# Kernel tuning notes

Hardware: AMD Instinct MI355X
Metric: run time of the kernel (lower is better)

Reference implementation:

```python
import jax, jax.numpy as jnp
import numpy as np

S, B, I, H = 96, 32, 64, 256


def setup_inputs() -> dict:
    key = jax.random.key(0)
    ks = jax.random.split(key, 10)
    wscale = 1.0 / np.sqrt(H)
    xscale = 1.0 / np.sqrt(I)
    return {
        "x": jax.random.normal(ks[0], (S, B, I), dtype=jnp.float32),
        # nn.Linear convention: y = x @ W.T + b, W has shape (out, in)
        "W_fx": jax.random.normal(ks[1], (H, I), dtype=jnp.float32) * xscale,
        "b_fx": jax.random.normal(ks[2], (H,), dtype=jnp.float32) * xscale,
        "W_fh": jax.random.normal(ks[3], (H, H), dtype=jnp.float32) * wscale,
        "b_fh": jax.random.normal(ks[4], (H,), dtype=jnp.float32) * wscale,
        "W_cx": jax.random.normal(ks[5], (H, I), dtype=jnp.float32) * xscale,
        "b_cx": jax.random.normal(ks[6], (H,), dtype=jnp.float32) * xscale,
        "W_ch": jax.random.normal(ks[7], (H, H), dtype=jnp.float32) * wscale,
        "b_ch": jax.random.normal(ks[8], (H,), dtype=jnp.float32) * wscale,
    }


def reference(x, W_fx, b_fx, W_fh, b_fh, W_cx, b_cx, W_ch, b_ch):
    """Faithful translation of the (buggy) torch forward.

    All three gates are the same sigmoid(f_x(x[t]) + f_h(h)) -- original reuses
    f_x/f_h for input/output gates. The candidate uses c_x(x) on the FULL
    sequence (not x[t]), so state broadcasts to (S, B, H) and h_seq is
    (S, S, B, H). Initial zero h/c are pre-broadcast to (S, B, H); since they
    are zeros this yields identical values to torch's scalar-shape init.
    """
    s, b, _ = x.shape
    h = W_fh.shape[0]
    # precompute the input projections once (same math, loop-invariant)
    fx = jnp.einsum('sbi,hi->sbh', x, W_fx) + b_fx   # (S,B,H), per-step slice
    cx = jnp.einsum('sbi,hi->sbh', x, W_cx) + b_cx   # (S,B,H), used whole every step (bug)

    def step(carry, fx_t):
        hh, cc = carry                                # each (S,B,H)
        g = jax.nn.sigmoid(fx_t + jnp.einsum('sbh,kh->sbk', hh, W_fh) + b_fh)
        cand = jnp.tanh(cx + jnp.einsum('sbh,kh->sbk', hh, W_ch) + b_ch)
        cc = g * cc + g * cand                        # forget==input gate
        hh = g * jnp.tanh(cc)                         # output gate == g
        return (hh, cc), hh

    h0 = jnp.zeros((s, b, h), dtype=x.dtype)
    (h_fin, c_fin), h_seq = jax.lax.scan(step, (h0, h0), fx)
    return h_seq, h_fin, c_fin
```

## Files before the change

kernel.cpp:

```cpp
#include <hip/hip_runtime.h>
#include <cmath>

#define S 96
#define BB 32
#define II 64
#define H 256
#define ROWS (S*BB)
#define R 16
#define NB (ROWS/R)
#define NT 512
#define PADK 272

#define FX_OFF 0
#define CX_OFF (ROWS*H)
#define WREP_OFF (2*ROWS*H)

typedef __attribute__((ext_vector_type(8))) _Float16 f16x8;
typedef __attribute__((ext_vector_type(4))) _Float16 f16x4;
typedef __attribute__((ext_vector_type(4))) float f32x4;
typedef unsigned short ushort_t;

__device__ inline ushort_t h2u(_Float16 h){ return __builtin_bit_cast(ushort_t, h); }

__device__ inline float sigm_fast(float x){
    return __builtin_amdgcn_rcpf(1.f + __expf(-x));
}
__device__ inline float tanh_fast(float x){
    return 1.f - 2.f*__builtin_amdgcn_rcpf(1.f + __expf(2.f*x));
}

__global__ void proj_kernel(const float* __restrict__ x,
                            const float* __restrict__ W_fx, const float* __restrict__ b_fx,
                            const float* __restrict__ W_cx, const float* __restrict__ b_cx,
                            const float* __restrict__ b_fh, const float* __restrict__ b_ch,
                            float* __restrict__ fx, float* __restrict__ cx)
{
    const int row = blockIdx.x;
    const int k = threadIdx.x;
    __shared__ float xs[II];
    if (k < II) xs[k] = x[row*II + k];
    __syncthreads();
    const float4* wf = reinterpret_cast<const float4*>(W_fx + k*II);
    const float4* wc = reinterpret_cast<const float4*>(W_cx + k*II);
    float af = 0.f, ac = 0.f;
#pragma unroll
    for (int i = 0; i < II/4; ++i) {
        float4 a = wf[i];
        float4 b = wc[i];
        const float* xp = &xs[i*4];
        af = fmaf(a.x, xp[0], fmaf(a.y, xp[1], fmaf(a.z, xp[2], fmaf(a.w, xp[3], af))));
        ac = fmaf(b.x, xp[0], fmaf(b.y, xp[1], fmaf(b.z, xp[2], fmaf(b.w, xp[3], ac))));
    }
    fx[row*H + k] = af + b_fx[k] + b_fh[k];
    cx[row*H + k] = ac + b_cx[k] + b_ch[k];
}

__global__ void repack_kernel(const float* __restrict__ Wf, const float* __restrict__ Wc,
                              ushort_t* __restrict__ wr)
{
    const int idx = blockIdx.x*256 + threadIdx.x;
    const int n = idx >> 8, k = idx & 255;
    const int lane = (((k >> 3) & 3) << 4) | (n & 15);
    const int dst = ((((n >> 4)*8 + (k >> 5))*64) + lane)*8 + (k & 7);
    wr[dst]         = h2u((_Float16)Wf[n*H + k]);
    wr[65536 + dst] = h2u((_Float16)Wc[n*H + k]);
}

__global__ __launch_bounds__(NT, 2) void lstm_mfma_kernel(
    const float* __restrict__ fx, const float* __restrict__ cx,
    const ushort_t* __restrict__ wr,
    float* __restrict__ out)
{
    const int tid = threadIdx.x;
    const int w = tid >> 6, lane = tid & 63;
    const int m = lane & 15, q = lane >> 4;
    const int b = blockIdx.x & 31;
    const int s0 = (blockIdx.x >> 5) * R;

    __shared__ ushort_t hh[2][2][R][PADK];

    for (int i = tid; i < 2*2*R*PADK; i += NT) (&hh[0][0][0][0])[i] = 0;

    f16x8 wF[2][8], wC[2][8];
#pragma unroll
    for (int ti = 0; ti < 2; ++ti)
#pragma unroll
        for (int kt = 0; kt < 8; ++kt) {
            const int fo = (((w*2 + ti)*8 + kt)*64 + lane)*8;
            wF[ti][kt] = *(const f16x8*)&wr[fo];
            wC[ti][kt] = *(const f16x8*)&wr[65536 + fo];
        }

    int col0[2];
    col0[0] = (w*2)*16 + q*4;
    col0[1] = (w*2 + 1)*16 + q*4;

    const int row = s0 + m;
    f32x4 cxr[2], cst[2];
#pragma unroll
    for (int ti = 0; ti < 2; ++ti) {
        cxr[ti] = *(const f32x4*)&cx[(row*BB + b)*H + col0[ti]];
        cst[ti] = (f32x4){0.f, 0.f, 0.f, 0.f};
    }

    float* hseq = out;
    float* hfin = out + (size_t)S*ROWS*H;
    float* cfin = hfin + (size_t)ROWS*H;

    const float* fxp = fx + b*H;
    float* op[2];
#pragma unroll
    for (int ti = 0; ti < 2; ++ti)
        op[ti] = hseq + ((size_t)row*BB + b)*H + col0[ti];

    __syncthreads();

    f32x4 fxv[2] = { *(const f32x4*)&fxp[col0[0]], *(const f32x4*)&fxp[col0[1]] };

#define LSTM_MFMA_TI(P, ti, accFti, accCti) do { \
    _Pragma("unroll") \
    for (int kt = 0; kt < 8; ++kt) { \
        f16x8 aH = *(const f16x8*)&hh[P][0][m][kt*32 + q*8]; \
        f16x8 aL = *(const f16x8*)&hh[P][1][m][kt*32 + q*8]; \
        accFti = __builtin_amdgcn_mfma_f32_16x16x32_f16(wF[ti][kt], aH, accFti, 0, 0, 0); \
        accFti = __builtin_amdgcn_mfma_f32_16x16x32_f16(wF[ti][kt], aL, accFti, 0, 0, 0); \
        accCti = __builtin_amdgcn_mfma_f32_16x16x32_f16(wC[ti][kt], aH, accCti, 0, 0, 0); \
        accCti = __builtin_amdgcn_mfma_f32_16x16x32_f16(wC[ti][kt], aL, accCti, 0, 0, 0); \
    } \
} while (0)

#define LSTM_EW_TI(P, ti, accFti, accCti, IS_LAST) do { \
    f32x4 hnv, cnv; \
    _Pragma("unroll") \
    for (int j = 0; j < 4; ++j) { \
        const float g    = sigm_fast(accFti[j] + fxv[ti][j]); \
        const float cand = tanh_fast(accCti[j] + cxr[ti][j]); \
        const float cn = g*(cst[ti][j] + cand); \
        cnv[j] = cn; \
        hnv[j] = g*tanh_fast(cn); \
    } \
    cst[ti] = cnv; \
    *(f32x4*)op[ti] = hnv; op[ti] += (size_t)S*BB*H; \
    f16x4 hi4, lo4; \
    _Pragma("unroll") \
    for (int j = 0; j < 4; ++j) { \
        hi4[j] = (_Float16)hnv[j]; \
        lo4[j] = (_Float16)(hnv[j] - (float)hi4[j]); \
    } \
    *(f16x4*)&hh[(P)^1][0][m][col0[ti]] = hi4; \
    *(f16x4*)&hh[(P)^1][1][m][col0[ti]] = lo4; \
    if (IS_LAST) { \
        const size_t ro = ((size_t)row*BB + b)*H + col0[ti]; \
        *(f32x4*)&hfin[ro] = hnv; \
        *(f32x4*)&cfin[ro] = cnv; \
    } \
} while (0)

#define LSTM_STEP(P, IS_LAST) do { \
    f32x4 accF0 = (f32x4){0.f,0.f,0.f,0.f}, accC0 = (f32x4){0.f,0.f,0.f,0.f}; \
    f32x4 accF1 = (f32x4){0.f,0.f,0.f,0.f}, accC1 = (f32x4){0.f,0.f,0.f,0.f}; \
    LSTM_MFMA_TI(P, 0, accF0, accC0); \
    LSTM_MFMA_TI(P, 1, accF1, accC1); \
    fxp += BB*H;    \
    f32x4 fxn0 = *(const f32x4*)&fxp[col0[0]]; \
    f32x4 fxn1 = *(const f32x4*)&fxp[col0[1]]; \
    LSTM_EW_TI(P, 0, accF0, accC0, IS_LAST);    \
    LSTM_EW_TI(P, 1, accF1, accC1, IS_LAST); \
    fxv[0] = fxn0; fxv[1] = fxn1; \
    asm volatile("s_waitcnt lgkmcnt(0)" ::: "memory"); \
    __builtin_amdgcn_s_barrier(); \
    asm volatile("" ::: "memory"); \
} while (0)

    for (int t = 0; t < S-2; t += 2) {
        LSTM_STEP(0, 0);
        LSTM_STEP(1, 0);
    }
    LSTM_STEP(0, 0);
    LSTM_STEP(1, 1);

#undef LSTM_STEP
#undef LSTM_EW_TI
#undef LSTM_MFMA_TI
}

extern "C" void kernel_launch(void* const* d_in, const int* in_sizes, int n_in,
                              void* d_out, int out_size, void* d_ws, size_t ws_size,
                              hipStream_t stream)
{
    const float* x    = (const float*)d_in[0];
    const float* W_fx = (const float*)d_in[1];
    const float* b_fx = (const float*)d_in[2];
    const float* W_fh = (const float*)d_in[3];
    const float* b_fh = (const float*)d_in[4];
    const float* W_cx = (const float*)d_in[5];
    const float* b_cx = (const float*)d_in[6];
    const float* W_ch = (const float*)d_in[7];
    const float* b_ch = (const float*)d_in[8];
    float* out = (float*)d_out;
    float* ws  = (float*)d_ws;

    float* fx = ws + FX_OFF;
    float* cx = ws + CX_OFF;
    ushort_t* wrp = (ushort_t*)(ws + WREP_OFF);

    hipLaunchKernelGGL(proj_kernel, dim3(ROWS), dim3(H), 0, stream,
                       x, W_fx, b_fx, W_cx, b_cx, b_fh, b_ch, fx, cx);
    hipLaunchKernelGGL(repack_kernel, dim3(H*H/256), dim3(256), 0, stream,
                       W_fh, W_ch, wrp);
    hipLaunchKernelGGL(lstm_mfma_kernel, dim3(NB), dim3(NT), 0, stream,
                       fx, cx, wrp, out);
}
```

Before: 503.4 us.

## Split LSTM recurrence across 16 waves and batch 16 rows per projection block

The recurrent kernel now uses 1024 threads so each wave owns one 16-column output tile instead of two. This halves per-wave weight registers and MFMA chain length and allows more waves per CU. The MFMA accumulators are seeded with the fx/cx projections, which removes the separate bias adds, and the F/C MFMAs are interleaved so the two dependency chains overlap. The projection kernel now handles 16 rows per block so each weight load is reused across rows, at the cost of larger per-thread register arrays and more barrier participants per step.

```diff
diff --git a/kernel.cpp b/kernel.cpp
--- a/kernel.cpp
+++ b/kernel.cpp
@@ -8,7 +8,7 @@
 #define ROWS (S*BB)
 #define R 16
 #define NB (ROWS/R)
-#define NT 512
+#define NT 1024
 #define PADK 272
 
 #define FX_OFF 0
@@ -29,30 +29,46 @@
     return 1.f - 2.f*__builtin_amdgcn_rcpf(1.f + __expf(2.f*x));
 }
 
-__global__ void proj_kernel(const float* __restrict__ x,
-                            const float* __restrict__ W_fx, const float* __restrict__ b_fx,
-                            const float* __restrict__ W_cx, const float* __restrict__ b_cx,
-                            const float* __restrict__ b_fh, const float* __restrict__ b_ch,
-                            float* __restrict__ fx, float* __restrict__ cx)
-{
-    const int row = blockIdx.x;
-    const int k = threadIdx.x;
-    __shared__ float xs[II];
-    if (k < II) xs[k] = x[row*II + k];
+__global__ __launch_bounds__(H) void proj_kernel(
+    const float* __restrict__ x,
+    const float* __restrict__ W_fx, const float* __restrict__ b_fx,
+    const float* __restrict__ W_cx, const float* __restrict__ b_cx,
+    const float* __restrict__ b_fh, const float* __restrict__ b_ch,
+    float* __restrict__ fx, float* __restrict__ cx)
+{
+    const int r0 = blockIdx.x * 16;
+    const int k  = threadIdx.x;
+
+    __shared__ float xs[16][II];
+    {
+        float4 v = reinterpret_cast<const float4*>(x + r0*II)[k];
+        reinterpret_cast<float4*>(&xs[0][0])[k] = v;
+    }
     __syncthreads();
+
     const float4* wf = reinterpret_cast<const float4*>(W_fx + k*II);
     const float4* wc = reinterpret_cast<const float4*>(W_cx + k*II);
-    float af = 0.f, ac = 0.f;
+    float af[16], ac[16];
+#pragma unroll
+    for (int r = 0; r < 16; ++r) { af[r] = 0.f; ac[r] = 0.f; }
 #pragma unroll
     for (int i = 0; i < II/4; ++i) {
-        float4 a = wf[i];
-        float4 b = wc[i];
-        const float* xp = &xs[i*4];
-        af = fmaf(a.x, xp[0], fmaf(a.y, xp[1], fmaf(a.z, xp[2], fmaf(a.w, xp[3], af))));
-        ac = fmaf(b.x, xp[0], fmaf(b.y, xp[1], fmaf(b.z, xp[2], fmaf(b.w, xp[3], ac))));
-    }
-    fx[row*H + k] = af + b_fx[k] + b_fh[k];
-    cx[row*H + k] = ac + b_cx[k] + b_ch[k];
+        const float4 a = wf[i];
+        const float4 b = wc[i];
+#pragma unroll
+        for (int r = 0; r < 16; ++r) {
+            const float* xp = &xs[r][i*4];
+            af[r] = fmaf(a.x, xp[0], fmaf(a.y, xp[1], fmaf(a.z, xp[2], fmaf(a.w, xp[3], af[r]))));
+            ac[r] = fmaf(b.x, xp[0], fmaf(b.y, xp[1], fmaf(b.z, xp[2], fmaf(b.w, xp[3], ac[r]))));
+        }
+    }
+    const float bf = b_fx[k] + b_fh[k];
+    const float bc = b_cx[k] + b_ch[k];
+#pragma unroll
+    for (int r = 0; r < 16; ++r) {
+        fx[(r0 + r)*H + k] = af[r] + bf;
+        cx[(r0 + r)*H + k] = ac[r] + bc;
+    }
 }
 
 __global__ void repack_kernel(const float* __restrict__ Wf, const float* __restrict__ Wc,
@@ -66,7 +82,7 @@
     wr[65536 + dst] = h2u((_Float16)Wc[n*H + k]);
 }
 
-__global__ __launch_bounds__(NT, 2) void lstm_mfma_kernel(
+__global__ __launch_bounds__(NT, 4) void lstm_mfma_kernel(
     const float* __restrict__ fx, const float* __restrict__ cx,
     const ushort_t* __restrict__ wr,
     float* __restrict__ out)
@@ -81,92 +97,70 @@
 
     for (int i = tid; i < 2*2*R*PADK; i += NT) (&hh[0][0][0][0])[i] = 0;
 
-    f16x8 wF[2][8], wC[2][8];
-#pragma unroll
-    for (int ti = 0; ti < 2; ++ti)
-#pragma unroll
-        for (int kt = 0; kt < 8; ++kt) {
-            const int fo = (((w*2 + ti)*8 + kt)*64 + lane)*8;
-            wF[ti][kt] = *(const f16x8*)&wr[fo];
-            wC[ti][kt] = *(const f16x8*)&wr[65536 + fo];
-        }
-
-    int col0[2];
-    col0[0] = (w*2)*16 + q*4;
-    col0[1] = (w*2 + 1)*16 + q*4;
-
-    const int row = s0 + m;
-    f32x4 cxr[2], cst[2];
-#pragma unroll
-    for (int ti = 0; ti < 2; ++ti) {
-        cxr[ti] = *(const f32x4*)&cx[(row*BB + b)*H + col0[ti]];
-        cst[ti] = (f32x4){0.f, 0.f, 0.f, 0.f};
-    }
+    f16x8 wF[8], wC[8];
+#pragma unroll
+    for (int kt = 0; kt < 8; ++kt) {
+        const int fo = ((w*8 + kt)*64 + lane)*8;
+        wF[kt] = *(const f16x8*)&wr[fo];
+        wC[kt] = *(const f16x8*)&wr[65536 + fo];
+    }
+
+    const int col0 = w*16 + q*4;
+    const int row  = s0 + m;
+
+    f32x4 cxr = *(const f32x4*)&cx[(row*BB + b)*H + col0];
+    f32x4 cst = (f32x4){0.f, 0.f, 0.f, 0.f};
 
     float* hseq = out;
     float* hfin = out + (size_t)S*ROWS*H;
     float* cfin = hfin + (size_t)ROWS*H;
 
-    const float* fxp = fx + b*H;
-    float* op[2];
-#pragma unroll
-    for (int ti = 0; ti < 2; ++ti)
-        op[ti] = hseq + ((size_t)row*BB + b)*H + col0[ti];
+    const float* fxp = fx + b*H + col0;
+    float* op = hseq + ((size_t)row*BB + b)*H + col0;
 
     __syncthreads();
 
-    f32x4 fxv[2] = { *(const f32x4*)&fxp[col0[0]], *(const f32x4*)&fxp[col0[1]] };
-
-#define LSTM_MFMA_TI(P, ti, accFti, accCti) do { \
+    f32x4 fxv = *(const f32x4*)fxp;
+
+#define LSTM_STEP(P, IS_LAST) do { \
+    f32x4 accF = fxv;       \
+    f32x4 accC = cxr;       \
     _Pragma("unroll") \
     for (int kt = 0; kt < 8; ++kt) { \
         f16x8 aH = *(const f16x8*)&hh[P][0][m][kt*32 + q*8]; \
         f16x8 aL = *(const f16x8*)&hh[P][1][m][kt*32 + q*8]; \
-        accFti = __builtin_amdgcn_mfma_f32_16x16x32_f16(wF[ti][kt], aH, accFti, 0, 0, 0); \
-        accFti = __builtin_amdgcn_mfma_f32_16x16x32_f16(wF[ti][kt], aL, accFti, 0, 0, 0); \
-        accCti = __builtin_amdgcn_mfma_f32_16x16x32_f16(wC[ti][kt], aH, accCti, 0, 0, 0); \
-        accCti = __builtin_amdgcn_mfma_f32_16x16x32_f16(wC[ti][kt], aL, accCti, 0, 0, 0); \
-    } \
-} while (0)
-
-#define LSTM_EW_TI(P, ti, accFti, accCti, IS_LAST) do { \
+        accF = __builtin_amdgcn_mfma_f32_16x16x32_f16(wF[kt], aH, accF, 0, 0, 0); \
+        accC = __builtin_amdgcn_mfma_f32_16x16x32_f16(wC[kt], aH, accC, 0, 0, 0); \
+        accF = __builtin_amdgcn_mfma_f32_16x16x32_f16(wF[kt], aL, accF, 0, 0, 0); \
+        accC = __builtin_amdgcn_mfma_f32_16x16x32_f16(wC[kt], aL, accC, 0, 0, 0); \
+    } \
+    fxp += BB*H;    \
+    f32x4 fxn = *(const f32x4*)fxp; \
     f32x4 hnv, cnv; \
     _Pragma("unroll") \
     for (int j = 0; j < 4; ++j) { \
-        const float g    = sigm_fast(accFti[j] + fxv[ti][j]); \
-        const float cand = tanh_fast(accCti[j] + cxr[ti][j]); \
-        const float cn = g*(cst[ti][j] + cand); \
+        const float g    = sigm_fast(accF[j]); \
+        const float cand = tanh_fast(accC[j]); \
+        const float cn = g*(cst[j] + cand); \
         cnv[j] = cn; \
         hnv[j] = g*tanh_fast(cn); \
     } \
-    cst[ti] = cnv; \
-    *(f32x4*)op[ti] = hnv; op[ti] += (size_t)S*BB*H; \
+    cst = cnv; \
+    *(f32x4*)op = hnv; op += (size_t)S*BB*H; \
     f16x4 hi4, lo4; \
     _Pragma("unroll") \
     for (int j = 0; j < 4; ++j) { \
         hi4[j] = (_Float16)hnv[j]; \
         lo4[j] = (_Float16)(hnv[j] - (float)hi4[j]); \
     } \
-    *(f16x4*)&hh[(P)^1][0][m][col0[ti]] = hi4; \
-    *(f16x4*)&hh[(P)^1][1][m][col0[ti]] = lo4; \
+    *(f16x4*)&hh[(P)^1][0][m][col0] = hi4; \
+    *(f16x4*)&hh[(P)^1][1][m][col0] = lo4; \
     if (IS_LAST) { \
-        const size_t ro = ((size_t)row*BB + b)*H + col0[ti]; \
+        const size_t ro = ((size_t)row*BB + b)*H + col0; \
         *(f32x4*)&hfin[ro] = hnv; \
         *(f32x4*)&cfin[ro] = cnv; \
     } \
-} while (0)
-
-#define LSTM_STEP(P, IS_LAST) do { \
-    f32x4 accF0 = (f32x4){0.f,0.f,0.f,0.f}, accC0 = (f32x4){0.f,0.f,0.f,0.f}; \
-    f32x4 accF1 = (f32x4){0.f,0.f,0.f,0.f}, accC1 = (f32x4){0.f,0.f,0.f,0.f}; \
-    LSTM_MFMA_TI(P, 0, accF0, accC0); \
-    LSTM_MFMA_TI(P, 1, accF1, accC1); \
-    fxp += BB*H;    \
-    f32x4 fxn0 = *(const f32x4*)&fxp[col0[0]]; \
-    f32x4 fxn1 = *(const f32x4*)&fxp[col0[1]]; \
-    LSTM_EW_TI(P, 0, accF0, accC0, IS_LAST);    \
-    LSTM_EW_TI(P, 1, accF1, accC1, IS_LAST); \
-    fxv[0] = fxn0; fxv[1] = fxn1; \
+    fxv = fxn; \
     asm volatile("s_waitcnt lgkmcnt(0)" ::: "memory"); \
     __builtin_amdgcn_s_barrier(); \
     asm volatile("" ::: "memory"); \
@@ -180,8 +174,6 @@
     LSTM_STEP(1, 1);
 
 #undef LSTM_STEP
-#undef LSTM_EW_TI
-#undef LSTM_MFMA_TI
 }
 
 extern "C" void kernel_launch(void* const* d_in, const int* in_sizes, int n_in,
@@ -204,7 +196,7 @@
     float* cx = ws + CX_OFF;
     ushort_t* wrp = (ushort_t*)(ws + WREP_OFF);
 
-    hipLaunchKernelGGL(proj_kernel, dim3(ROWS), dim3(H), 0, stream,
+    hipLaunchKernelGGL(proj_kernel, dim3(NB), dim3(H), 0, stream,
                        x, W_fx, b_fx, W_cx, b_cx, b_fh, b_ch, fx, cx);
     hipLaunchKernelGGL(repack_kernel, dim3(H*H/256), dim3(256), 0, stream,
                        W_fh, W_ch, wrp);
```

New measurement: 431.6 us. -14.3%, faster.
